# Kernel tuning notes

Measured on AMD Instinct MI355X. Metric: run time of the kernel, lower is better.

The kernel has to match this reference:

```python
import jax, jax.numpy as jnp
import numpy as np

C = 128          # in_channels
NODE_NUM = 8192  # number of unique source nodes this step
D = 64           # max_member_num (fixed degree -> neighbor_bool all True)
E = NODE_NUM * D # total gathered neighbor slots
N_TOTAL = 200000 # total nodes in graph
NEG_SLOPE = 0.2


def setup_inputs() -> dict:
    key = jax.random.key(0)
    ks = jax.random.split(key, 8)
    node_features = jax.random.normal(ks[0], (N_TOTAL, C), jnp.float32)
    memory = jax.random.normal(ks[1], (N_TOTAL, C), jnp.float32)
    sc = 1.0 / np.sqrt(C)
    W_max = jax.random.normal(ks[2], (C, C), jnp.float32) * sc
    b_max = jnp.zeros((C,), jnp.float32)
    W_score = jax.random.normal(ks[3], (2 * C, 1), jnp.float32) * (1.0 / np.sqrt(2 * C))
    b_score = jnp.zeros((1,), jnp.float32)
    W_fit = jax.random.normal(ks[4], (C, 1), jnp.float32) * sc
    b_fit = jnp.zeros((1,), jnp.float32)
    neighbors = jax.random.randint(ks[5], (E,), 0, N_TOTAL)  # gathered neighbor node ids
    seg = jnp.repeat(jnp.arange(NODE_NUM), D)                # index_source_nodes (segment ids)
    return dict(node_features=node_features, memory=memory, W_max=W_max, b_max=b_max,
                W_score=W_score, b_score=b_score, W_fit=W_fit, b_fit=b_fit,
                neighbors=neighbors, seg=seg)


def reference(node_features, memory, W_max, b_max, W_score, b_score, W_fit, b_fit, neighbors, seg):
    # gather: features + detached memory per neighbor slot  [E, C]
    nbr = node_features[neighbors] + jax.lax.stop_gradient(memory[neighbors])
    # scatter_max per source node, then linear + re-gather duplication
    max_feature = jax.ops.segment_max(nbr, seg, num_segments=NODE_NUM)      # [node_num, C]
    max_lin = max_feature @ W_max + b_max                                    # [node_num, C]
    dup = max_lin[seg]                                                       # [E, C]
    # attention score over concat(center_max, neighbor)
    s = jnp.concatenate([dup, nbr], axis=-1) @ W_score + b_score             # [E, 1]
    s = jnp.where(s >= 0, s, NEG_SLOPE * s)                                  # leaky_relu
    # segment softmax over neighbors of each source node
    smax = jax.ops.segment_max(s, seg, num_segments=NODE_NUM)[seg]
    ex = jnp.exp(s - smax)
    denom = jax.ops.segment_sum(ex, seg, num_segments=NODE_NUM)[seg]
    score = ex / denom                                                       # [E, 1]
    # masked scatter into fixed [node_num, max_member_num] tensor (full mask -> reshape)
    score_tensor = score.reshape(NODE_NUM, D)
    # scatter_add pooling of score-weighted neighbor features
    cluster_feature = jax.ops.segment_sum(nbr * score, seg, num_segments=NODE_NUM)  # [node_num, C]
    # community fitness via linear score calculator + sigmoid
    fitness = jax.nn.sigmoid(cluster_feature @ W_fit + b_fit).reshape(-1)    # [node_num]
    return cluster_feature, score_tensor, fitness
```

## Files before the change

### kernel.cpp

```cpp
#include <hip/hip_runtime.h>
#include <math.h>

#define C_DIM 128
#define DQ 32
#define DEG 64
#define NODES 8192
#define NEG_SLOPE 0.2f

__global__ void precompute_kernel(const float* __restrict__ W_max,
                                  const float* __restrict__ b_max,
                                  const float* __restrict__ W_score,
                                  const float* __restrict__ b_score,
                                  float* __restrict__ ws) {
    const int c = threadIdx.x;
    float acc = 0.f;
    #pragma unroll 4
    for (int k = 0; k < C_DIM; ++k)
        acc += W_max[c * C_DIM + k] * W_score[k];
    ws[c] = acc;

    __shared__ float red[C_DIM];
    red[c] = b_max[c] * W_score[c];
    __syncthreads();
    for (int off = 64; off > 0; off >>= 1) {
        if (c < off) red[c] += red[c + off];
        __syncthreads();
    }
    if (c == 0) ws[C_DIM] = red[0] + b_score[0];
}

__global__ __launch_bounds__(256)
void detector_kernel(const float* __restrict__ nf,
                     const float* __restrict__ mem,
                     const float* __restrict__ W_score,
                     const float* __restrict__ W_fit,
                     const float* __restrict__ b_fit,
                     const int* __restrict__ neighbors,
                     const float* __restrict__ ws,
                     float* __restrict__ out_cf,
                     float* __restrict__ out_score,
                     float* __restrict__ out_fit) {
    __shared__ float4 red[256];
    __shared__ float  s_raw[DEG];
    __shared__ float  sc[DEG];
    __shared__ int    s_nb[DEG];
    __shared__ float  t1_sh;

    const int tid = threadIdx.x;
    const int n   = blockIdx.x;
    const int q   = tid & 31;
    const int g   = tid >> 5;

    if (tid < DEG) s_nb[tid] = neighbors[n * DEG + tid];
    const float4 wsb = ((const float4*)(W_score + C_DIM))[q];
    __syncthreads();

    const float4* nf4  = (const float4*)nf;
    const float4* mem4 = (const float4*)mem;

    float4 v[8];
    float4 mx = make_float4(-INFINITY, -INFINITY, -INFINITY, -INFINITY);

    #pragma unroll
    for (int i = 0; i < 8; ++i) {
        const int j = i * 8 + g;
        const int node = s_nb[j];
        const float4 a = nf4[(long)node * DQ + q];
        const float4 b = mem4[(long)node * DQ + q];
        float4 vv;
        vv.x = a.x + b.x; vv.y = a.y + b.y; vv.z = a.z + b.z; vv.w = a.w + b.w;
        v[i] = vv;
        mx.x = fmaxf(mx.x, vv.x); mx.y = fmaxf(mx.y, vv.y);
        mx.z = fmaxf(mx.z, vv.z); mx.w = fmaxf(mx.w, vv.w);
        float p = vv.x * wsb.x + vv.y * wsb.y + vv.z * wsb.z + vv.w * wsb.w;
        p += __shfl_xor(p, 1);
        p += __shfl_xor(p, 2);
        p += __shfl_xor(p, 4);
        p += __shfl_xor(p, 8);
        p += __shfl_xor(p, 16);
        if (q == 0) s_raw[j] = p;
    }
    red[tid] = mx;
    __syncthreads();

    if (tid < 32) {
        float4 f = red[tid];
        #pragma unroll
        for (int r = 1; r < 8; ++r) {
            const float4 o = red[tid + 32 * r];
            f.x = fmaxf(f.x, o.x); f.y = fmaxf(f.y, o.y);
            f.z = fmaxf(f.z, o.z); f.w = fmaxf(f.w, o.w);
        }
        const float4 wc = ((const float4*)ws)[tid];
        float t1 = f.x * wc.x + f.y * wc.y + f.z * wc.z + f.w * wc.w;
        t1 += __shfl_xor(t1, 1);
        t1 += __shfl_xor(t1, 2);
        t1 += __shfl_xor(t1, 4);
        t1 += __shfl_xor(t1, 8);
        t1 += __shfl_xor(t1, 16);
        if (tid == 0) t1_sh = t1 + ws[C_DIM];
    }
    __syncthreads();

    if (tid < DEG) {
        float s = t1_sh + s_raw[tid];
        s = (s >= 0.f) ? s : NEG_SLOPE * s;
        float m = s;
        #pragma unroll
        for (int msk = 1; msk <= 32; msk <<= 1)
            m = fmaxf(m, __shfl_xor(m, msk));
        const float ex = __expf(s - m);
        float d = ex;
        #pragma unroll
        for (int msk = 1; msk <= 32; msk <<= 1)
            d += __shfl_xor(d, msk);
        const float sv = ex / d;
        sc[tid] = sv;
        out_score[n * DEG + tid] = sv;
    }
    __syncthreads();

    float4 acc = make_float4(0.f, 0.f, 0.f, 0.f);
    #pragma unroll
    for (int i = 0; i < 8; ++i) {
        const float w = sc[i * 8 + g];
        acc.x += v[i].x * w; acc.y += v[i].y * w;
        acc.z += v[i].z * w; acc.w += v[i].w * w;
    }
    red[tid] = acc;
    __syncthreads();

    if (tid < 32) {
        float4 f = red[tid];
        #pragma unroll
        for (int r = 1; r < 8; ++r) {
            const float4 o = red[tid + 32 * r];
            f.x += o.x; f.y += o.y; f.z += o.z; f.w += o.w;
        }
        ((float4*)(out_cf + (long)n * C_DIM))[tid] = f;
        const float4 wf = ((const float4*)W_fit)[tid];
        float fp = f.x * wf.x + f.y * wf.y + f.z * wf.z + f.w * wf.w;
        fp += __shfl_xor(fp, 1);
        fp += __shfl_xor(fp, 2);
        fp += __shfl_xor(fp, 4);
        fp += __shfl_xor(fp, 8);
        fp += __shfl_xor(fp, 16);
        if (tid == 0)
            out_fit[n] = 1.f / (1.f + __expf(-(fp + b_fit[0])));
    }
}

extern "C" void kernel_launch(void* const* d_in, const int* in_sizes, int n_in,
                              void* d_out, int out_size, void* d_ws, size_t ws_size,
                              hipStream_t stream) {
    const float* node_features = (const float*)d_in[0];
    const float* memory        = (const float*)d_in[1];
    const float* W_max         = (const float*)d_in[2];
    const float* b_max         = (const float*)d_in[3];
    const float* W_score       = (const float*)d_in[4];
    const float* b_score       = (const float*)d_in[5];
    const float* W_fit         = (const float*)d_in[6];
    const float* b_fit         = (const float*)d_in[7];
    const int*   neighbors     = (const int*)d_in[8];

    float* ws = (float*)d_ws;
    float* out_cf    = (float*)d_out;
    float* out_score = out_cf + (long)NODES * C_DIM;
    float* out_fit   = out_score + (long)NODES * DEG;

    precompute_kernel<<<1, C_DIM, 0, stream>>>(W_max, b_max, W_score, b_score, ws);
    detector_kernel<<<NODES, 256, 0, stream>>>(node_features, memory, W_score,
                                               W_fit, b_fit, neighbors, ws,
                                               out_cf, out_score, out_fit);
}
```

Before: 269.7 us.

## Pre-sum features and memory into a workspace table before the neighbor gather

A new streaming kernel adds node_features and memory element-wise into a single workspace table. The weight-combination precompute now runs in block 0 of that same kernel, so it needs no separate launch. The detector then gathers one row per neighbor instead of two, which halves random gather requests and makes the gathered table smaller and more cache-friendly. In exchange it adds a full sequential read of both tables plus a write of the summed table, and it only runs when the workspace is large enough. Neighbor ids are now loaded with vector int4 reads per thread group, which removes a shared-memory staging step and a barrier.

```diff
diff --git a/kernel.cpp b/kernel.cpp
--- a/kernel.cpp
+++ b/kernel.cpp
@@ -4,46 +4,58 @@
 #define C_DIM 128
 #define DQ 32
 #define DEG 64
-#define NODES 8192
 #define NEG_SLOPE 0.2f
 
-__global__ void precompute_kernel(const float* __restrict__ W_max,
-                                  const float* __restrict__ b_max,
-                                  const float* __restrict__ W_score,
-                                  const float* __restrict__ b_score,
-                                  float* __restrict__ ws) {
-    const int c = threadIdx.x;
-    float acc = 0.f;
-    #pragma unroll 4
-    for (int k = 0; k < C_DIM; ++k)
-        acc += W_max[c * C_DIM + k] * W_score[k];
-    ws[c] = acc;
-
-    __shared__ float red[C_DIM];
-    red[c] = b_max[c] * W_score[c];
-    __syncthreads();
-    for (int off = 64; off > 0; off >>= 1) {
-        if (c < off) red[c] += red[c + off];
+__global__ __launch_bounds__(256)
+void fuse_sum_kernel(const float4* __restrict__ nf4,
+                     const float4* __restrict__ mem4,
+                     float4* __restrict__ sum4, long n4,
+                     const float* __restrict__ W_max,
+                     const float* __restrict__ b_max,
+                     const float* __restrict__ W_score,
+                     const float* __restrict__ b_score,
+                     float* __restrict__ combo) {
+    const long stride = (long)gridDim.x * 256;
+    for (long i = (long)blockIdx.x * 256 + threadIdx.x; i < n4; i += stride) {
+        const float4 a = nf4[i];
+        const float4 b = mem4[i];
+        sum4[i] = make_float4(a.x + b.x, a.y + b.y, a.z + b.z, a.w + b.w);
+    }
+    if (blockIdx.x == 0) {
+        const int c = threadIdx.x;
+        __shared__ float red[C_DIM];
+        if (c < C_DIM) {
+            float acc = 0.f;
+            #pragma unroll 4
+            for (int k = 0; k < C_DIM; ++k)
+                acc += W_max[c * C_DIM + k] * W_score[k];
+            combo[c] = acc;
+            red[c] = b_max[c] * W_score[c];
+        }
         __syncthreads();
-    }
-    if (c == 0) ws[C_DIM] = red[0] + b_score[0];
-}
-
+        for (int off = 64; off > 0; off >>= 1) {
+            if (c < off) red[c] += red[c + off];
+            __syncthreads();
+        }
+        if (c == 0) combo[C_DIM] = red[0] + b_score[0];
+    }
+}
+
+template <bool FUSED>
 __global__ __launch_bounds__(256)
-void detector_kernel(const float* __restrict__ nf,
+void detector_kernel(const float* __restrict__ src,
                      const float* __restrict__ mem,
                      const float* __restrict__ W_score,
                      const float* __restrict__ W_fit,
                      const float* __restrict__ b_fit,
                      const int* __restrict__ neighbors,
-                     const float* __restrict__ ws,
+                     const float* __restrict__ combo,
                      float* __restrict__ out_cf,
                      float* __restrict__ out_score,
                      float* __restrict__ out_fit) {
     __shared__ float4 red[256];
     __shared__ float  s_raw[DEG];
     __shared__ float  sc[DEG];
-    __shared__ int    s_nb[DEG];
     __shared__ float  t1_sh;
 
     const int tid = threadIdx.x;
@@ -51,11 +63,14 @@
     const int q   = tid & 31;
     const int g   = tid >> 5;
 
-    if (tid < DEG) s_nb[tid] = neighbors[n * DEG + tid];
+    const int4* nb4 = (const int4*)(neighbors + n * DEG + g * 8);
+    const int4 nba = nb4[0];
+    const int4 nbb = nb4[1];
+    const int ids[8] = {nba.x, nba.y, nba.z, nba.w, nbb.x, nbb.y, nbb.z, nbb.w};
+
     const float4 wsb = ((const float4*)(W_score + C_DIM))[q];
-    __syncthreads();
-
-    const float4* nf4  = (const float4*)nf;
+
+    const float4* src4 = (const float4*)src;
     const float4* mem4 = (const float4*)mem;
 
     float4 v[8];
@@ -63,12 +78,13 @@
 
     #pragma unroll
     for (int i = 0; i < 8; ++i) {
-        const int j = i * 8 + g;
-        const int node = s_nb[j];
-        const float4 a = nf4[(long)node * DQ + q];
-        const float4 b = mem4[(long)node * DQ + q];
-        float4 vv;
-        vv.x = a.x + b.x; vv.y = a.y + b.y; vv.z = a.z + b.z; vv.w = a.w + b.w;
+        const int j = g * 8 + i;
+        const long node = ids[i];
+        float4 vv = src4[node * DQ + q];
+        if (!FUSED) {
+            const float4 b = mem4[node * DQ + q];
+            vv.x += b.x; vv.y += b.y; vv.z += b.z; vv.w += b.w;
+        }
         v[i] = vv;
         mx.x = fmaxf(mx.x, vv.x); mx.y = fmaxf(mx.y, vv.y);
         mx.z = fmaxf(mx.z, vv.z); mx.w = fmaxf(mx.w, vv.w);
@@ -80,6 +96,8 @@
         p += __shfl_xor(p, 16);
         if (q == 0) s_raw[j] = p;
     }
+    asm volatile("" ::: "memory");
+
     red[tid] = mx;
     __syncthreads();
 
@@ -91,14 +109,14 @@
             f.x = fmaxf(f.x, o.x); f.y = fmaxf(f.y, o.y);
             f.z = fmaxf(f.z, o.z); f.w = fmaxf(f.w, o.w);
         }
-        const float4 wc = ((const float4*)ws)[tid];
+        const float4 wc = ((const float4*)combo)[tid];
         float t1 = f.x * wc.x + f.y * wc.y + f.z * wc.z + f.w * wc.w;
         t1 += __shfl_xor(t1, 1);
         t1 += __shfl_xor(t1, 2);
         t1 += __shfl_xor(t1, 4);
         t1 += __shfl_xor(t1, 8);
         t1 += __shfl_xor(t1, 16);
-        if (tid == 0) t1_sh = t1 + ws[C_DIM];
+        if (tid == 0) t1_sh = t1 + combo[C_DIM];
     }
     __syncthreads();
 
@@ -123,7 +141,7 @@
     float4 acc = make_float4(0.f, 0.f, 0.f, 0.f);
     #pragma unroll
     for (int i = 0; i < 8; ++i) {
-        const float w = sc[i * 8 + g];
+        const float w = sc[g * 8 + i];
         acc.x += v[i].x * w; acc.y += v[i].y * w;
         acc.z += v[i].z * w; acc.w += v[i].w * w;
     }
@@ -148,6 +166,27 @@
         if (tid == 0)
             out_fit[n] = 1.f / (1.f + __expf(-(fp + b_fit[0])));
     }
+}
+
+__global__ void precompute_kernel(const float* __restrict__ W_max,
+                                  const float* __restrict__ b_max,
+                                  const float* __restrict__ W_score,
+                                  const float* __restrict__ b_score,
+                                  float* __restrict__ combo) {
+    const int c = threadIdx.x;
+    float acc = 0.f;
+    #pragma unroll 4
+    for (int k = 0; k < C_DIM; ++k)
+        acc += W_max[c * C_DIM + k] * W_score[k];
+    combo[c] = acc;
+    __shared__ float red[C_DIM];
+    red[c] = b_max[c] * W_score[c];
+    __syncthreads();
+    for (int off = 64; off > 0; off >>= 1) {
+        if (c < off) red[c] += red[c + off];
+        __syncthreads();
+    }
+    if (c == 0) combo[C_DIM] = red[0] + b_score[0];
 }
 
 extern "C" void kernel_launch(void* const* d_in, const int* in_sizes, int n_in,
@@ -163,13 +202,31 @@
     const float* b_fit         = (const float*)d_in[7];
     const int*   neighbors     = (const int*)d_in[8];
 
-    float* ws = (float*)d_ws;
+    const long n_total  = in_sizes[0] / C_DIM;
+    const long n_elem   = (long)in_sizes[0];
+    const int  nodes    = in_sizes[8] / DEG;
+    const long n4       = n_elem / 4;
+
+    float* combo = (float*)d_ws;
+    float* sum   = combo + 512;
+    const size_t need = (size_t)(512 + n_elem) * sizeof(float);
+
     float* out_cf    = (float*)d_out;
-    float* out_score = out_cf + (long)NODES * C_DIM;
-    float* out_fit   = out_score + (long)NODES * DEG;
-
-    precompute_kernel<<<1, C_DIM, 0, stream>>>(W_max, b_max, W_score, b_score, ws);
-    detector_kernel<<<NODES, 256, 0, stream>>>(node_features, memory, W_score,
-                                               W_fit, b_fit, neighbors, ws,
-                                               out_cf, out_score, out_fit);
-}
+    float* out_score = out_cf + (long)nodes * C_DIM;
+    float* out_fit   = out_score + (long)nodes * DEG;
+
+    if (ws_size >= need) {
+        fuse_sum_kernel<<<4096, 256, 0, stream>>>(
+            (const float4*)node_features, (const float4*)memory,
+            (float4*)sum, n4, W_max, b_max, W_score, b_score, combo);
+        detector_kernel<true><<<nodes, 256, 0, stream>>>(
+            sum, nullptr, W_score, W_fit, b_fit, neighbors, combo,
+            out_cf, out_score, out_fit);
+    } else {
+        precompute_kernel<<<1, C_DIM, 0, stream>>>(W_max, b_max, W_score,
+                                                   b_score, combo);
+        detector_kernel<false><<<nodes, 256, 0, stream>>>(
+            node_features, memory, W_score, W_fit, b_fit, neighbors, combo,
+            out_cf, out_score, out_fit);
+    }
+}
```

Result: slower. 292.0 us (+8.3%).
